# Performance work log

Measured on AMD Instinct MI355X. Metric: run time of the kernel, lower is better.

The kernel has to match this reference:

```python
import jax, jax.numpy as jnp
import numpy as np

N_GAUSS = 4096
M_POINTS = 65536
EPS = 1e-6


def setup_inputs() -> dict:
    key = jax.random.key(0)
    k1, k2, k3, k4, k5 = jax.random.split(key, 5)
    sample_points = jax.random.uniform(k1, (M_POINTS, 3), dtype=jnp.float32)
    positions = jax.random.uniform(k2, (N_GAUSS, 3), dtype=jnp.float32)
    # realistic Gaussian widths around initial_scale = 0.1 / N^(1/3)
    scales = 0.05 + 0.10 * jax.random.uniform(k3, (N_GAUSS, 3), dtype=jnp.float32)
    rotations = jax.random.normal(k4, (N_GAUSS, 4), dtype=jnp.float32)
    intensities = 0.5 * jax.random.uniform(k5, (N_GAUSS,), dtype=jnp.float32)
    return {
        "sample_points": sample_points,
        "positions": positions,
        "scales": scales,
        "rotations": rotations,
        "intensities": intensities,
    }


def _quat_to_rotmat(quats):
    # quats: (N,4) -> (N,3,3), matches torch module's normalization (+1e-8)
    q = quats / (jnp.linalg.norm(quats, axis=1, keepdims=True) + 1e-8)
    w, x, y, z = q[:, 0], q[:, 1], q[:, 2], q[:, 3]
    R = jnp.stack([
        jnp.stack([1 - 2 * (y * y + z * z), 2 * (x * y - z * w), 2 * (x * z + y * w)], axis=-1),
        jnp.stack([2 * (x * y + z * w), 1 - 2 * (x * x + z * z), 2 * (y * z - x * w)], axis=-1),
        jnp.stack([2 * (x * z - y * w), 2 * (y * z + x * w), 1 - 2 * (x * x + y * y)], axis=-1),
    ], axis=-2)
    return R  # (N,3,3)


def reference(sample_points, positions, scales, rotations, intensities):
    # f(x_m) = sum_n w_n * exp(-0.5 * (x_m - mu_n)^T A_n (x_m - mu_n)),
    # A_n = R_n diag(1/s_n^2) R_n^T  (inverse covariance)
    s = jnp.abs(scales) + EPS                              # (N,3)
    R = _quat_to_rotmat(rotations)                         # (N,3,3)
    inv_s2 = 1.0 / (s * s)                                 # (N,3)
    A = jnp.einsum('nij,nj,nkj->nik', R, inv_s2, R)        # (N,3,3)
    b = jnp.einsum('nij,nj->ni', A, positions)             # (N,3)
    c = jnp.einsum('ni,ni->n', b, positions)               # (N,)
    M = sample_points.shape[0]
    X2 = (sample_points[:, :, None] * sample_points[:, None, :]).reshape(M, 9)  # (M,9)
    Aflat = A.reshape(-1, 9)                               # (N,9)
    # (M,N) Mahalanobis distances via two GEMMs (no (M,N,3) intermediate)
    q = X2 @ Aflat.T - 2.0 * (sample_points @ b.T) + c[None, :]
    out = jnp.exp(-0.5 * q) @ intensities                  # (M,)
    return out
```

## Files before the change

kernel.cpp:

```cpp
#include <hip/hip_runtime.h>


#define M_POINTS 65536
#define N_GAUSS  4096
#define KNEG     (-0.72134752044448170f)

typedef _Float16 half8   __attribute__((ext_vector_type(8)));
typedef float    float4v __attribute__((ext_vector_type(4)));
typedef float    v2f     __attribute__((ext_vector_type(2)));

__device__ __forceinline__ float fast_exp2(float x) {
#if defined(__has_builtin)
#if __has_builtin(__builtin_amdgcn_exp2f)
    return __builtin_amdgcn_exp2f(x);
#else
    return exp2f(x);
#endif
#else
    return exp2f(x);
#endif
}

__global__ __launch_bounds__(256) void precompute_bfrag(
    const float* __restrict__ pos, const float* __restrict__ scl,
    const float* __restrict__ rot, const float* __restrict__ inten,
    half8* __restrict__ bfrag, float4* __restrict__ out_zero)
{
    int n = blockIdx.x * 256 + threadIdx.x;
    if (n >= N_GAUSS) return;

    {
        float4 z = make_float4(0.f, 0.f, 0.f, 0.f);
        out_zero[n]         = z;
        out_zero[n + 4096]  = z;
        out_zero[n + 8192]  = z;
        out_zero[n + 12288] = z;
    }

    float qw = rot[4*n+0], qx = rot[4*n+1], qy = rot[4*n+2], qz = rot[4*n+3];
    float nrm = sqrtf(qw*qw + qx*qx + qy*qy + qz*qz) + 1e-8f;
    float ir = 1.0f / nrm;
    qw *= ir; qx *= ir; qy *= ir; qz *= ir;

    float r00 = 1.f - 2.f*(qy*qy + qz*qz);
    float r01 = 2.f*(qx*qy - qz*qw);
    float r02 = 2.f*(qx*qz + qy*qw);
    float r10 = 2.f*(qx*qy + qz*qw);
    float r11 = 1.f - 2.f*(qx*qx + qz*qz);
    float r12 = 2.f*(qy*qz - qx*qw);
    float r20 = 2.f*(qx*qz - qy*qw);
    float r21 = 2.f*(qy*qz + qx*qw);
    float r22 = 1.f - 2.f*(qx*qx + qy*qy);

    float s0 = fabsf(scl[3*n+0]) + 1e-6f;
    float s1 = fabsf(scl[3*n+1]) + 1e-6f;
    float s2 = fabsf(scl[3*n+2]) + 1e-6f;
    float w0 = 1.f/(s0*s0), w1 = 1.f/(s1*s1), w2 = 1.f/(s2*s2);

    float a00 = r00*r00*w0 + r01*r01*w1 + r02*r02*w2;
    float a01 = r00*r10*w0 + r01*r11*w1 + r02*r12*w2;
    float a02 = r00*r20*w0 + r01*r21*w1 + r02*r22*w2;
    float a11 = r10*r10*w0 + r11*r11*w1 + r12*r12*w2;
    float a12 = r10*r20*w0 + r11*r21*w1 + r12*r22*w2;
    float a22 = r20*r20*w0 + r21*r21*w1 + r22*r22*w2;

    float p0 = pos[3*n+0], p1 = pos[3*n+1], p2 = pos[3*n+2];
    float b0 = a00*p0 + a01*p1 + a02*p2;
    float b1 = a01*p0 + a11*p1 + a12*p2;
    float b2 = a02*p0 + a12*p1 + a22*p2;
    float c  = b0*p0 + b1*p1 + b2*p2;

    float I = fmaxf(inten[n], 1e-30f);

    float C[10];
    C[0] = KNEG * a00;       C[1] = KNEG * a11;       C[2] = KNEG * a22;
    C[3] = 2.f*KNEG * a01;   C[4] = 2.f*KNEG * a02;   C[5] = 2.f*KNEG * a12;
    C[6] = -2.f*KNEG * b0;   C[7] = -2.f*KNEG * b1;   C[8] = -2.f*KNEG * b2;
    C[9] = KNEG * c + log2f(I);

    _Float16 chi[10], clo[10];
#pragma unroll
    for (int j = 0; j < 10; ++j) {
        chi[j] = (_Float16)C[j];
        clo[j] = (_Float16)(C[j] - (float)chi[j]);
    }

    const int tile = n >> 4, nl = n & 15;
#pragma unroll
    for (int q = 0; q < 4; ++q) {
        half8 v;
#pragma unroll
        for (int j = 0; j < 8; ++j) {
            const int k = q*8 + j;
            _Float16 h = (_Float16)0.f;
            if (k < 30) {
                const int jm = k / 3, s = k % 3;
                h = (s == 2) ? clo[jm] : chi[jm];
            }
            v[j] = h;
        }
        bfrag[tile*64 + q*16 + nl] = v;
    }
}

__device__ __forceinline__ half8 build_afrag(float x, float y, float z, int q) {
    const float P0 = x*x, P1 = y*y, P2 = z*z;
    const float P3 = x*y, P4 = x*z, P5 = y*z;

    _Float16 h0 = (_Float16)P0, l0 = (_Float16)(P0 - (float)h0);
    _Float16 h1 = (_Float16)P1, l1 = (_Float16)(P1 - (float)h1);
    _Float16 h2 = (_Float16)P2, l2 = (_Float16)(P2 - (float)h2);
    _Float16 h3 = (_Float16)P3, l3 = (_Float16)(P3 - (float)h3);
    _Float16 h4 = (_Float16)P4, l4 = (_Float16)(P4 - (float)h4);
    _Float16 h5 = (_Float16)P5, l5 = (_Float16)(P5 - (float)h5);
    _Float16 h6 = (_Float16)x,  l6 = (_Float16)(x - (float)h6);
    _Float16 h7 = (_Float16)y,  l7 = (_Float16)(y - (float)h7);
    _Float16 h8 = (_Float16)z,  l8 = (_Float16)(z - (float)h8);
    const _Float16 one = (_Float16)1.f, zer = (_Float16)0.f;

    half8 c0 = {h0, l0, h0, h1, l1, h1, h2, l2};
    half8 c1 = {h2, h3, l3, h3, h4, l4, h4, h5};
    half8 c2 = {l5, h5, h6, l6, h6, h7, l7, h7};
    half8 c3 = {h8, l8, h8, one, zer, one, zer, zer};

    return (q == 0) ? c0 : (q == 1) ? c1 : (q == 2) ? c2 : c3;
}

#define PT_SLABS  512
#define G_SPLIT   4
#define G_TILES   (256 / G_SPLIT)

__global__ __launch_bounds__(256) void gauss_eval(
    const float* __restrict__ pts,
    const half8* __restrict__ bfrag,
    float* __restrict__ out)
{
    const int tid  = threadIdx.x;
    const int lane = tid & 63;
    const int wv   = tid >> 6;
    const int ml   = lane & 15;
    const int q    = lane >> 4;

    const int base = blockIdx.x * 128 + wv * 32;

    const int p0i = base + ml, p1i = base + 16 + ml;
    half8 af0 = build_afrag(pts[3*p0i], pts[3*p0i+1], pts[3*p0i+2], q);
    half8 af1 = build_afrag(pts[3*p1i], pts[3*p1i+1], pts[3*p1i+2], q);

    v2f a0lo = {0.f, 0.f}, a0hi = {0.f, 0.f};
    v2f a1lo = {0.f, 0.f}, a1hi = {0.f, 0.f};
    const float4v zero4 = {0.f, 0.f, 0.f, 0.f};

    const half8* src = bfrag + (blockIdx.y * G_TILES) * 64 + lane;

#pragma unroll 4
    for (int i = 0; i < G_TILES; ++i) {
        half8 b = src[i * 64];
        float4v d0 = __builtin_amdgcn_mfma_f32_16x16x32_f16(af0, b, zero4, 0, 0, 0);
        float4v d1 = __builtin_amdgcn_mfma_f32_16x16x32_f16(af1, b, zero4, 0, 0, 0);
        v2f e0lo = { fast_exp2(d0[0]), fast_exp2(d0[1]) };
        v2f e0hi = { fast_exp2(d0[2]), fast_exp2(d0[3]) };
        v2f e1lo = { fast_exp2(d1[0]), fast_exp2(d1[1]) };
        v2f e1hi = { fast_exp2(d1[2]), fast_exp2(d1[3]) };
        a0lo += e0lo;
        a0hi += e0hi;
        a1lo += e1lo;
        a1hi += e1hi;
    }

#pragma unroll
    for (int m = 1; m <= 8; m <<= 1) {
        v2f t0lo = { __shfl_xor(a0lo.x, m), __shfl_xor(a0lo.y, m) };
        v2f t0hi = { __shfl_xor(a0hi.x, m), __shfl_xor(a0hi.y, m) };
        v2f t1lo = { __shfl_xor(a1lo.x, m), __shfl_xor(a1lo.y, m) };
        v2f t1hi = { __shfl_xor(a1hi.x, m), __shfl_xor(a1hi.y, m) };
        a0lo += t0lo; a0hi += t0hi; a1lo += t1lo; a1hi += t1hi;
    }

    if (ml == 0) {
        const int o = base + q*4;
        atomicAdd(&out[o + 0],  a0lo.x);
        atomicAdd(&out[o + 1],  a0lo.y);
        atomicAdd(&out[o + 2],  a0hi.x);
        atomicAdd(&out[o + 3],  a0hi.y);
        atomicAdd(&out[o + 16], a1lo.x);
        atomicAdd(&out[o + 17], a1lo.y);
        atomicAdd(&out[o + 18], a1hi.x);
        atomicAdd(&out[o + 19], a1hi.y);
    }
}

extern "C" void kernel_launch(void* const* d_in, const int* in_sizes, int n_in,
                              void* d_out, int out_size, void* d_ws, size_t ws_size,
                              hipStream_t stream) {
    const float* sample_points = (const float*)d_in[0];
    const float* positions     = (const float*)d_in[1];
    const float* scales        = (const float*)d_in[2];
    const float* rotations     = (const float*)d_in[3];
    const float* intensities   = (const float*)d_in[4];

    half8* bfrag = (half8*)d_ws;

    precompute_bfrag<<<N_GAUSS / 256, 256, 0, stream>>>(
        positions, scales, rotations, intensities, bfrag, (float4*)d_out);

    gauss_eval<<<dim3(PT_SLABS, G_SPLIT), 256, 0, stream>>>(
        sample_points, bfrag, (float*)d_out);
}
```

Before: 99.99 us.

## Switch Gaussian evaluation to 32x32x16 MFMA tiles with 32-Gaussian fragments

Reorganizes the B-fragment layout into 32-Gaussian tiles and replaces the pair of 16x16x32 MFMAs per tile with two chained 32x32x16 MFMAs covering the 32-wide K dimension. Each wave now handles 32 points against 32 Gaussians per iteration, producing 16 accumulator values per lane, with a wider shuffle reduction and 16 atomics per reducing lane. The aim is to cut MFMA issue count and B-fragment loads per useful output, at the cost of more live registers and a longer cross-lane reduction.

```diff
diff --git a/kernel.cpp b/kernel.cpp
--- a/kernel.cpp
+++ b/kernel.cpp
@@ -5,9 +5,8 @@
 #define N_GAUSS  4096
 #define KNEG     (-0.72134752044448170f)
 
-typedef _Float16 half8   __attribute__((ext_vector_type(8)));
-typedef float    float4v __attribute__((ext_vector_type(4)));
-typedef float    v2f     __attribute__((ext_vector_type(2)));
+typedef _Float16 half8    __attribute__((ext_vector_type(8)));
+typedef float    float16v __attribute__((ext_vector_type(16)));
 
 __device__ __forceinline__ float fast_exp2(float x) {
 #if defined(__has_builtin)
@@ -85,13 +84,13 @@
         clo[j] = (_Float16)(C[j] - (float)chi[j]);
     }
 
-    const int tile = n >> 4, nl = n & 15;
-#pragma unroll
-    for (int q = 0; q < 4; ++q) {
+    const int tile = n >> 5, nl = n & 31;
+#pragma unroll
+    for (int o = 0; o < 4; ++o) {
         half8 v;
 #pragma unroll
         for (int j = 0; j < 8; ++j) {
-            const int k = q*8 + j;
+            const int k = o*8 + j;
             _Float16 h = (_Float16)0.f;
             if (k < 30) {
                 const int jm = k / 3, s = k % 3;
@@ -99,11 +98,11 @@
             }
             v[j] = h;
         }
-        bfrag[tile*64 + q*16 + nl] = v;
-    }
-}
-
-__device__ __forceinline__ half8 build_afrag(float x, float y, float z, int q) {
+        bfrag[tile*128 + o*32 + nl] = v;
+    }
+}
+
+__device__ __forceinline__ half8 build_afrag(float x, float y, float z, int o) {
     const float P0 = x*x, P1 = y*y, P2 = z*z;
     const float P3 = x*y, P4 = x*z, P5 = y*z;
 
@@ -123,12 +122,12 @@
     half8 c2 = {l5, h5, h6, l6, h6, h7, l7, h7};
     half8 c3 = {h8, l8, h8, one, zer, one, zer, zer};
 
-    return (q == 0) ? c0 : (q == 1) ? c1 : (q == 2) ? c2 : c3;
-}
-
-#define PT_SLABS  512
+    return (o == 0) ? c0 : (o == 1) ? c1 : (o == 2) ? c2 : c3;
+}
+
+#define PT_BLOCKS 512
 #define G_SPLIT   4
-#define G_TILES   (256 / G_SPLIT)
+#define NT        (128 / G_SPLIT)
 
 __global__ __launch_bounds__(256) void gauss_eval(
     const float* __restrict__ pts,
@@ -138,55 +137,49 @@
     const int tid  = threadIdx.x;
     const int lane = tid & 63;
     const int wv   = tid >> 6;
-    const int ml   = lane & 15;
-    const int q    = lane >> 4;
-
-    const int base = blockIdx.x * 128 + wv * 32;
-
-    const int p0i = base + ml, p1i = base + 16 + ml;
-    half8 af0 = build_afrag(pts[3*p0i], pts[3*p0i+1], pts[3*p0i+2], q);
-    half8 af1 = build_afrag(pts[3*p1i], pts[3*p1i+1], pts[3*p1i+2], q);
-
-    v2f a0lo = {0.f, 0.f}, a0hi = {0.f, 0.f};
-    v2f a1lo = {0.f, 0.f}, a1hi = {0.f, 0.f};
-    const float4v zero4 = {0.f, 0.f, 0.f, 0.f};
-
-    const half8* src = bfrag + (blockIdx.y * G_TILES) * 64 + lane;
-
-#pragma unroll 4
-    for (int i = 0; i < G_TILES; ++i) {
-        half8 b = src[i * 64];
-        float4v d0 = __builtin_amdgcn_mfma_f32_16x16x32_f16(af0, b, zero4, 0, 0, 0);
-        float4v d1 = __builtin_amdgcn_mfma_f32_16x16x32_f16(af1, b, zero4, 0, 0, 0);
-        v2f e0lo = { fast_exp2(d0[0]), fast_exp2(d0[1]) };
-        v2f e0hi = { fast_exp2(d0[2]), fast_exp2(d0[3]) };
-        v2f e1lo = { fast_exp2(d1[0]), fast_exp2(d1[1]) };
-        v2f e1hi = { fast_exp2(d1[2]), fast_exp2(d1[3]) };
-        a0lo += e0lo;
-        a0hi += e0hi;
-        a1lo += e1lo;
-        a1hi += e1hi;
-    }
-
-#pragma unroll
-    for (int m = 1; m <= 8; m <<= 1) {
-        v2f t0lo = { __shfl_xor(a0lo.x, m), __shfl_xor(a0lo.y, m) };
-        v2f t0hi = { __shfl_xor(a0hi.x, m), __shfl_xor(a0hi.y, m) };
-        v2f t1lo = { __shfl_xor(a1lo.x, m), __shfl_xor(a1lo.y, m) };
-        v2f t1hi = { __shfl_xor(a1hi.x, m), __shfl_xor(a1hi.y, m) };
-        a0lo += t0lo; a0hi += t0hi; a1lo += t1lo; a1hi += t1hi;
-    }
-
-    if (ml == 0) {
-        const int o = base + q*4;
-        atomicAdd(&out[o + 0],  a0lo.x);
-        atomicAdd(&out[o + 1],  a0lo.y);
-        atomicAdd(&out[o + 2],  a0hi.x);
-        atomicAdd(&out[o + 3],  a0hi.y);
-        atomicAdd(&out[o + 16], a1lo.x);
-        atomicAdd(&out[o + 17], a1lo.y);
-        atomicAdd(&out[o + 18], a1hi.x);
-        atomicAdd(&out[o + 19], a1hi.y);
+    const int nl   = lane & 31;
+    const int h    = lane >> 5;
+
+    const int pbase = (blockIdx.x * 4 + wv) * 32;
+    const int pt = pbase + nl;
+    const float x = pts[3*pt+0], y = pts[3*pt+1], z = pts[3*pt+2];
+
+    const half8 af1 = build_afrag(x, y, z, h);
+    const half8 af2 = build_afrag(x, y, z, 2 + h);
+
+    float16v acc = {0.f,0.f,0.f,0.f,0.f,0.f,0.f,0.f,
+                    0.f,0.f,0.f,0.f,0.f,0.f,0.f,0.f};
+    const float16v zero16 = {0.f,0.f,0.f,0.f,0.f,0.f,0.f,0.f,
+                             0.f,0.f,0.f,0.f,0.f,0.f,0.f,0.f};
+
+    const half8* src = bfrag + (blockIdx.y * NT) * 128 + lane;
+
+#pragma unroll 2
+    for (int i = 0; i < NT; ++i) {
+        half8 b1 = src[i*128];
+        half8 b2 = src[i*128 + 64];
+        float16v d = __builtin_amdgcn_mfma_f32_32x32x16_f16(af1, b1, zero16, 0, 0, 0);
+        d = __builtin_amdgcn_mfma_f32_32x32x16_f16(af2, b2, d, 0, 0, 0);
+        float16v e;
+#pragma unroll
+        for (int r = 0; r < 16; ++r) e[r] = fast_exp2(d[r]);
+        acc += e;
+    }
+
+#pragma unroll
+    for (int m = 1; m <= 16; m <<= 1) {
+        float16v t;
+#pragma unroll
+        for (int r = 0; r < 16; ++r) t[r] = __shfl_xor(acc[r], m);
+        acc += t;
+    }
+
+    if (nl == 0) {
+#pragma unroll
+        for (int r = 0; r < 16; ++r) {
+            const int row = (r & 3) + 8 * (r >> 2) + 4 * h;
+            atomicAdd(&out[pbase + row], acc[r]);
+        }
     }
 }
 
@@ -204,6 +197,6 @@
     precompute_bfrag<<<N_GAUSS / 256, 256, 0, stream>>>(
         positions, scales, rotations, intensities, bfrag, (float4*)d_out);
 
-    gauss_eval<<<dim3(PT_SLABS, G_SPLIT), 256, 0, stream>>>(
+    gauss_eval<<<dim3(PT_BLOCKS, G_SPLIT), 256, 0, stream>>>(
         sample_points, bfrag, (float*)d_out);
 }
```

Result: no change. 100.2 us (+0.2%).
